# Kernel optimization log

Hardware: AMD Instinct MI355X
Metric: run time of the kernel (lower is better)

Reference implementation:

```python
import jax, jax.numpy as jnp
import numpy as np

N, E, D = 40000, 640000, 128
EPS = 1e-5


def _lin(k, out_d, in_d):
    s = 1.0 / np.sqrt(in_d)
    kw, kb = jax.random.split(k)
    W = jax.random.uniform(kw, (out_d, in_d), minval=-s, maxval=s, dtype=jnp.float32)
    b = jax.random.uniform(kb, (out_d,), minval=-s, maxval=s, dtype=jnp.float32)
    return W, b


def setup_inputs() -> dict:
    key = jax.random.key(0)
    kx, ke, k1, k2, k3, k4 = jax.random.split(key, 6)
    x = jax.random.normal(kx, (N, D), dtype=jnp.float32)
    edge_index = jax.random.randint(ke, (2, E), 0, N, dtype=jnp.int64)
    Wm1, bm1 = _lin(k1, D, D)
    Wm2, bm2 = _lin(k2, D, D)
    Wu1, bu1 = _lin(k3, D, 2 * D)
    Wu2, bu2 = _lin(k4, D, D)
    gamma = jnp.ones((D,), jnp.float32)
    beta = jnp.zeros((D,), jnp.float32)
    return dict(x=x, edge_index=edge_index, Wm1=Wm1, bm1=bm1, Wm2=Wm2, bm2=bm2,
                Wu1=Wu1, bu1=bu1, Wu2=Wu2, bu2=bu2, gamma=gamma, beta=beta)


def reference(x, edge_index, Wm1, bm1, Wm2, bm2, Wu1, bu1, Wu2, bu2, gamma, beta):
    num_nodes = x.shape[0]
    src, dst = edge_index[0], edge_index[1]
    # message MLP on gathered source features: (E, D)
    m = jax.nn.relu(x[src] @ Wm1.T + bm1) @ Wm2.T + bm2
    # scatter-mean via segment_sum + clamped count
    agg = jax.ops.segment_sum(m, dst, num_segments=num_nodes)
    cnt = jax.ops.segment_sum(jnp.ones((dst.shape[0],), m.dtype), dst, num_segments=num_nodes)
    agg = agg / jnp.clip(cnt, 1.0, None)[:, None]
    # update MLP on concat([x, agg]) -> (N, D); dropout is identity in eval
    comb = jnp.concatenate([x, agg], axis=-1)
    u = jax.nn.relu(comb @ Wu1.T + bu1) @ Wu2.T + bu2
    # residual + LayerNorm
    h = u + x
    mu = h.mean(-1, keepdims=True)
    var = ((h - mu) ** 2).mean(-1, keepdims=True)
    return (h - mu) / jnp.sqrt(var + EPS) * gamma + beta
```

## Files before the change

kernel.cpp:

```cpp
#include <hip/hip_runtime.h>

#define N_NODES 40000
#define N_EDGES 640000
#define DIM 128
#define PAD 64
#define NBLK_GEMM 313

typedef __bf16 bf16;
typedef __bf16 v8bf __attribute__((ext_vector_type(8)));
typedef __bf16 v4bf __attribute__((ext_vector_type(4)));
typedef float f32x4 __attribute__((ext_vector_type(4)));

#define MFMA(a, b, c) __builtin_amdgcn_mfma_f32_16x16x32_bf16(a, b, c, 0, 0, 0)

#define OFF_WM1 0
#define OFF_BM1 16384
#define OFF_WM2 16512
#define OFF_BM2 32896
#define OFF_WU1 33024
#define OFF_BU1 65792
#define OFF_WU2 65920
#define OFF_BU2 82304
#define OFF_GAM 82432
#define OFF_BET 82560
#define NPARAM  82688

__global__ __launch_bounds__(256) void front_kernel(
    const void* __restrict__ x, const void* __restrict__ ei,
    const void* p0, const void* p1, const void* p2, const void* p3,
    const void* p4, const void* p5, const void* p6, const void* p7,
    const void* p8, const void* p9,
    bf16* __restrict__ wp, bf16* __restrict__ xb,
    int* __restrict__ cnt, int* __restrict__ flags)
{
    __shared__ int sf[2];
    const int tid = threadIdx.x;
    const int gid = blockIdx.x * 256 + tid;
    const int gstride = gridDim.x * 256;

    if (tid == 0) { sf[0] = 0; sf[1] = 0; }
    __syncthreads();
    {
        const unsigned short* xh = (const unsigned short*)x;
        const unsigned int* eiw = (const unsigned int*)ei;
        int isf32 = 0; unsigned int orhi = 0;
        #pragma unroll
        for (int j = 0; j < 4; ++j) {
            unsigned short h = xh[2 * (tid + 256 * j)];
            if (((h >> 7) & 0xFF) >= 0xC0) isf32 = 1;
            orhi |= eiw[2 * (tid + 256 * j) + 1];
        }
        if (isf32) atomicOr(&sf[0], 1);
        if (orhi)  atomicOr(&sf[1], 1);
    }
    __syncthreads();
    const int f32m = sf[0];
    if (blockIdx.x == 0 && tid == 0) { flags[0] = f32m; flags[1] = sf[1] ? 0 : 1; }

    for (int i = gid; i < NPARAM; i += gstride) {
        const void* src; int base;
        if      (i < OFF_BM1) { src = p0; base = OFF_WM1; }
        else if (i < OFF_WM2) { src = p1; base = OFF_BM1; }
        else if (i < OFF_BM2) { src = p2; base = OFF_WM2; }
        else if (i < OFF_WU1) { src = p3; base = OFF_BM2; }
        else if (i < OFF_BU1) { src = p4; base = OFF_WU1; }
        else if (i < OFF_WU2) { src = p5; base = OFF_BU1; }
        else if (i < OFF_BU2) { src = p6; base = OFF_WU2; }
        else if (i < OFF_GAM) { src = p7; base = OFF_BU2; }
        else if (i < OFF_BET) { src = p8; base = OFF_GAM; }
        else                  { src = p9; base = OFF_BET; }
        int j = i - base;
        float v = f32m ? ((const float*)src)[j] : (float)((const bf16*)src)[j];
        wp[i] = (bf16)v;
    }
    {
        const int NT = N_NODES * DIM;
        if (f32m) {
            const float4* g = (const float4*)x;
            v4bf* o = (v4bf*)xb;
            for (int i = gid; i < NT / 4; i += gstride) {
                float4 v = g[i];
                v4bf t; t[0] = (bf16)v.x; t[1] = (bf16)v.y; t[2] = (bf16)v.z; t[3] = (bf16)v.w;
                o[i] = t;
            }
        } else {
            const uint4* g = (const uint4*)x;
            uint4* o = (uint4*)xb;
            for (int i = gid; i < NT / 8; i += gstride) o[i] = g[i];
        }
    }
    for (int i = gid; i < N_NODES; i += gstride) cnt[i] = 0;
}

__global__ __launch_bounds__(256) void scatter_kernel(const void* __restrict__ ei,
                                                      int* __restrict__ cnt,
                                                      int* __restrict__ padded,
                                                      const int* __restrict__ flags) {
    int e = blockIdx.x * 256 + threadIdx.x;
    if (e >= N_EDGES) return;
    int s, d;
    if (flags[1]) {
        const long long* p = (const long long*)ei;
        s = (int)p[e]; d = (int)p[N_EDGES + e];
    } else {
        const int* p = (const int*)ei;
        s = p[e]; d = p[N_EDGES + e];
    }
    int pos = atomicAdd(&cnt[d], 1);
    if (pos < PAD) padded[(d << 6) + pos] = s;
}

__global__ __launch_bounds__(256) void msg_kernel(const bf16* __restrict__ xb,
                                                  const bf16* __restrict__ wp,
                                                  bf16* __restrict__ y)
{
    __shared__ __align__(16) bf16 sc[4][32 * DIM];
    const int wave = threadIdx.x >> 6, lane = threadIdx.x & 63;
    const int l15 = lane & 15, quad = lane >> 4;
    const int row0 = (blockIdx.x * 4 + wave) * 32;
    bf16* s = sc[wave];
    const bf16* W1 = wp + OFF_WM1;
    const bf16* W2 = wp + OFF_WM2;

    const int ra = min(row0 + l15, N_NODES - 1);
    const int rb = min(row0 + 16 + l15, N_NODES - 1);

    f32x4 acc[2][8] = {};
    #pragma unroll
    for (int kt = 0; kt < 4; ++kt) {
        int k0 = kt * 32 + quad * 8;
        v8bf a0 = *(const v8bf*)&xb[(size_t)ra * DIM + k0];
        v8bf a1 = *(const v8bf*)&xb[(size_t)rb * DIM + k0];
        #pragma unroll
        for (int ct = 0; ct < 8; ++ct) {
            v8bf b = *(const v8bf*)&W1[(ct * 16 + l15) * DIM + k0];
            acc[0][ct] = MFMA(a0, b, acc[0][ct]);
            acc[1][ct] = MFMA(a1, b, acc[1][ct]);
        }
    }
    #pragma unroll
    for (int ct = 0; ct < 8; ++ct) {
        float bb = (float)wp[OFF_BM1 + ct * 16 + l15];
        int c8w = (ct << 1) | (l15 >> 3);
        #pragma unroll
        for (int i = 0; i < 2; ++i)
            #pragma unroll
            for (int r = 0; r < 4; ++r) {
                int row = i * 16 + quad * 4 + r;
                s[row * DIM + (((c8w ^ (row & 15)) << 3) | (l15 & 7))] =
                    (bf16)fmaxf(acc[i][ct][r] + bb, 0.f);
            }
    }
    f32x4 acc2[2][8] = {};
    #pragma unroll
    for (int kt = 0; kt < 4; ++kt) {
        int k0 = kt * 32 + quad * 8;
        int c8 = kt * 4 + quad;
        v8bf a0 = *(const v8bf*)&s[l15 * DIM + ((c8 ^ l15) << 3)];
        v8bf a1 = *(const v8bf*)&s[(16 + l15) * DIM + ((c8 ^ l15) << 3)];
        #pragma unroll
        for (int ct = 0; ct < 8; ++ct) {
            v8bf b = *(const v8bf*)&W2[(ct * 16 + l15) * DIM + k0];
            acc2[0][ct] = MFMA(a0, b, acc2[0][ct]);
            acc2[1][ct] = MFMA(a1, b, acc2[1][ct]);
        }
    }
    #pragma unroll
    for (int ct = 0; ct < 8; ++ct) {
        float bb = (float)wp[OFF_BM2 + ct * 16 + l15];
        #pragma unroll
        for (int i = 0; i < 2; ++i)
            #pragma unroll
            for (int r = 0; r < 4; ++r) {
                int grow = row0 + i * 16 + quad * 4 + r;
                if (grow < N_NODES)
                    y[(size_t)grow * DIM + ct * 16 + l15] = (bf16)(acc2[i][ct][r] + bb);
            }
    }
}

__global__ __launch_bounds__(256) void update_kernel(const bf16* __restrict__ xb,
                                                     const bf16* __restrict__ agg,
                                                     const bf16* __restrict__ wp,
                                                     const int* __restrict__ flags,
                                                     void* __restrict__ out)
{
    __shared__ __align__(16) bf16 sc[4][32 * DIM];
    const int wave = threadIdx.x >> 6, lane = threadIdx.x & 63;
    const int l15 = lane & 15, quad = lane >> 4;
    const int row0 = (blockIdx.x * 4 + wave) * 32;
    bf16* s = sc[wave];
    const bf16* W1 = wp + OFF_WU1;
    const bf16* W2 = wp + OFF_WU2;
    const int of32 = flags[0];

    const int ra = min(row0 + l15, N_NODES - 1);
    const int rb = min(row0 + 16 + l15, N_NODES - 1);

    f32x4 acc[2][8] = {};
    #pragma unroll
    for (int kt = 0; kt < 8; ++kt) {
        int k0 = kt * 32 + quad * 8;
        const bf16* A = (kt < 4) ? xb : agg;
        int ko = (kt < 4) ? k0 : (k0 - 128);
        v8bf a0 = *(const v8bf*)&A[(size_t)ra * DIM + ko];
        v8bf a1 = *(const v8bf*)&A[(size_t)rb * DIM + ko];
        #pragma unroll
        for (int ct = 0; ct < 8; ++ct) {
            v8bf b = *(const v8bf*)&W1[(ct * 16 + l15) * 256 + k0];
            acc[0][ct] = MFMA(a0, b, acc[0][ct]);
            acc[1][ct] = MFMA(a1, b, acc[1][ct]);
        }
    }
    #pragma unroll
    for (int ct = 0; ct < 8; ++ct) {
        float bb = (float)wp[OFF_BU1 + ct * 16 + l15];
        int c8w = (ct << 1) | (l15 >> 3);
        #pragma unroll
        for (int i = 0; i < 2; ++i)
            #pragma unroll
            for (int r = 0; r < 4; ++r) {
                int row = i * 16 + quad * 4 + r;
                s[row * DIM + (((c8w ^ (row & 15)) << 3) | (l15 & 7))] =
                    (bf16)fmaxf(acc[i][ct][r] + bb, 0.f);
            }
    }
    f32x4 acc2[2][8] = {};
    #pragma unroll
    for (int kt = 0; kt < 4; ++kt) {
        int k0 = kt * 32 + quad * 8;
        int c8 = kt * 4 + quad;
        v8bf a0 = *(const v8bf*)&s[l15 * DIM + ((c8 ^ l15) << 3)];
        v8bf a1 = *(const v8bf*)&s[(16 + l15) * DIM + ((c8 ^ l15) << 3)];
        #pragma unroll
        for (int ct = 0; ct < 8; ++ct) {
            v8bf b = *(const v8bf*)&W2[(ct * 16 + l15) * DIM + k0];
            acc2[0][ct] = MFMA(a0, b, acc2[0][ct]);
            acc2[1][ct] = MFMA(a1, b, acc2[1][ct]);
        }
    }

    float bu2c[8], gc[8], bc[8];
    #pragma unroll
    for (int ct = 0; ct < 8; ++ct) {
        int col = ct * 16 + l15;
        bu2c[ct] = (float)wp[OFF_BU2 + col];
        gc[ct]   = (float)wp[OFF_GAM + col];
        bc[ct]   = (float)wp[OFF_BET + col];
    }
    #pragma unroll
    for (int i = 0; i < 2; ++i) {
        #pragma unroll
        for (int r = 0; r < 4; ++r) {
            int grow = row0 + i * 16 + quad * 4 + r;
            int growc = min(grow, N_NODES - 1);
            float u[8], s1 = 0.f, s2 = 0.f;
            #pragma unroll
            for (int ct = 0; ct < 8; ++ct) {
                float v = acc2[i][ct][r] + bu2c[ct]
                        + (float)xb[(size_t)growc * DIM + ct * 16 + l15];
                u[ct] = v; s1 += v; s2 += v * v;
            }
            #pragma unroll
            for (int off = 1; off < 16; off <<= 1) {
                s1 += __shfl_xor(s1, off);
                s2 += __shfl_xor(s2, off);
            }
            float mean = s1 * (1.f / 128.f);
            float var  = s2 * (1.f / 128.f) - mean * mean;
            float rstd = rsqrtf(var + 1e-5f);
            if (grow < N_NODES) {
                if (of32) {
                    #pragma unroll
                    for (int ct = 0; ct < 8; ++ct)
                        ((float*)out)[(size_t)grow * DIM + ct * 16 + l15] =
                            (u[ct] - mean) * rstd * gc[ct] + bc[ct];
                } else {
                    #pragma unroll
                    for (int ct = 0; ct < 8; ++ct)
                        ((bf16*)out)[(size_t)grow * DIM + ct * 16 + l15] =
                            (bf16)((u[ct] - mean) * rstd * gc[ct] + bc[ct]);
                }
            }
        }
    }
}

__device__ __forceinline__ void accum8(float* s, uint4 v) {
    v8bf b = __builtin_bit_cast(v8bf, v);
    #pragma unroll
    for (int j = 0; j < 8; ++j) s[j] += (float)b[j];
}

__global__ __launch_bounds__(256) void agg_kernel(const bf16* __restrict__ y,
                                                  const int* __restrict__ padded,
                                                  const int* __restrict__ cnt,
                                                  bf16* __restrict__ agg) {
    const int node = (blockIdx.x << 2) + (threadIdx.x >> 6);
    const int lane = threadIdx.x & 63;
    const int slot = lane >> 4, c16 = lane & 15;
    const int c = min(cnt[node], PAD);
    const int beg = node << 6;
    const int end = beg + c;
    const uint4* yv = (const uint4*)y;

    float s0[8] = {}, s1[8] = {};
    int e = beg + slot;
    for (; e + 4 < end; e += 8) {
        int i0 = padded[e], i1 = padded[e + 4];
        uint4 v0 = yv[(size_t)i0 * 16 + c16];
        uint4 v1 = yv[(size_t)i1 * 16 + c16];
        accum8(s0, v0);
        accum8(s1, v1);
    }
    if (e < end) accum8(s0, yv[(size_t)padded[e] * 16 + c16]);

    float inv = 1.f / (float)(c > 0 ? c : 1);
    v8bf o;
    #pragma unroll
    for (int j = 0; j < 8; ++j) {
        float v = s0[j] + s1[j];
        v += __shfl_xor(v, 16);
        v += __shfl_xor(v, 32);
        o[j] = (bf16)(v * inv);
    }
    if (slot == 0)
        ((uint4*)agg)[(size_t)node * 16 + c16] = __builtin_bit_cast(uint4, o);
}

extern "C" void kernel_launch(void* const* d_in, const int* in_sizes, int n_in,
                              void* d_out, int out_size, void* d_ws, size_t ws_size,
                              hipStream_t stream) {
    const void* x  = d_in[0];
    const void* ei = d_in[1];

    char* ws = (char*)d_ws;
    size_t off = 0;
    auto alloc = [&](size_t bytes) {
        void* p = ws + off;
        off += (bytes + 255) & ~(size_t)255;
        return p;
    };
    bf16* y      = (bf16*)alloc((size_t)N_NODES * DIM * sizeof(bf16));
    bf16* agg    = (bf16*)alloc((size_t)N_NODES * DIM * sizeof(bf16));
    bf16* xb     = (bf16*)alloc((size_t)N_NODES * DIM * sizeof(bf16));
    bf16* wp     = (bf16*)alloc((size_t)NPARAM * sizeof(bf16));
    int*  cnt    = (int*)alloc(N_NODES * sizeof(int));
    int*  padded = (int*)alloc((size_t)N_NODES * PAD * sizeof(int));
    int*  flags  = (int*)alloc(256);

    front_kernel<<<1024, 256, 0, stream>>>(
        x, ei, d_in[2], d_in[3], d_in[4], d_in[5], d_in[6], d_in[7],
        d_in[8], d_in[9], d_in[10], d_in[11], wp, xb, cnt, flags);
    scatter_kernel<<<(N_EDGES + 255) / 256, 256, 0, stream>>>(ei, cnt, padded, flags);
    msg_kernel<<<NBLK_GEMM, 256, 0, stream>>>(xb, wp, y);
    agg_kernel<<<N_NODES / 4, 256, 0, stream>>>(y, padded, cnt, agg);
    update_kernel<<<NBLK_GEMM, 256, 0, stream>>>(xb, agg, wp, flags, d_out);
}
```

Before: 221.3 us.

## Fuse edge scatter with message MLP and drop the bf16 pre-conversion kernel

```diff
diff --git a/kernel.cpp b/kernel.cpp
--- a/kernel.cpp
+++ b/kernel.cpp
@@ -4,124 +4,63 @@
 #define N_EDGES 640000
 #define DIM 128
 #define PAD 64
-#define NBLK_GEMM 313
+#define NBLK_MSG 313
+#define FAT_BLOCKS (NBLK_MSG * 9)
 
 typedef __bf16 bf16;
 typedef __bf16 v8bf __attribute__((ext_vector_type(8)));
-typedef __bf16 v4bf __attribute__((ext_vector_type(4)));
 typedef float f32x4 __attribute__((ext_vector_type(4)));
 
 #define MFMA(a, b, c) __builtin_amdgcn_mfma_f32_16x16x32_bf16(a, b, c, 0, 0, 0)
 
-#define OFF_WM1 0
-#define OFF_BM1 16384
-#define OFF_WM2 16512
-#define OFF_BM2 32896
-#define OFF_WU1 33024
-#define OFF_BU1 65792
-#define OFF_WU2 65920
-#define OFF_BU2 82304
-#define OFF_GAM 82432
-#define OFF_BET 82560
-#define NPARAM  82688
-
-__global__ __launch_bounds__(256) void front_kernel(
-    const void* __restrict__ x, const void* __restrict__ ei,
-    const void* p0, const void* p1, const void* p2, const void* p3,
-    const void* p4, const void* p5, const void* p6, const void* p7,
-    const void* p8, const void* p9,
-    bf16* __restrict__ wp, bf16* __restrict__ xb,
-    int* __restrict__ cnt, int* __restrict__ flags)
-{
-    __shared__ int sf[2];
+__device__ __forceinline__ void detect(const void* x, const void* ei,
+                                       int* sf, int& f32m, int& i64m) {
     const int tid = threadIdx.x;
-    const int gid = blockIdx.x * 256 + tid;
-    const int gstride = gridDim.x * 256;
-
     if (tid == 0) { sf[0] = 0; sf[1] = 0; }
     __syncthreads();
-    {
-        const unsigned short* xh = (const unsigned short*)x;
-        const unsigned int* eiw = (const unsigned int*)ei;
-        int isf32 = 0; unsigned int orhi = 0;
-        #pragma unroll
-        for (int j = 0; j < 4; ++j) {
-            unsigned short h = xh[2 * (tid + 256 * j)];
-            if (((h >> 7) & 0xFF) >= 0xC0) isf32 = 1;
-            orhi |= eiw[2 * (tid + 256 * j) + 1];
-        }
-        if (isf32) atomicOr(&sf[0], 1);
-        if (orhi)  atomicOr(&sf[1], 1);
-    }
+    const unsigned short* xh = (const unsigned short*)x;
+    const unsigned int* eiw = (const unsigned int*)ei;
+    int isf32 = 0; unsigned int orhi = 0;
+    #pragma unroll
+    for (int j = 0; j < 4; ++j) {
+        unsigned short h = xh[2 * (tid + 256 * j)];
+        if (((h >> 7) & 0xFF) >= 0xC0) isf32 = 1;
+        orhi |= eiw[2 * (tid + 256 * j) + 1];
+    }
+    if (isf32) atomicOr(&sf[0], 1);
+    if (orhi)  atomicOr(&sf[1], 1);
     __syncthreads();
-    const int f32m = sf[0];
-    if (blockIdx.x == 0 && tid == 0) { flags[0] = f32m; flags[1] = sf[1] ? 0 : 1; }
-
-    for (int i = gid; i < NPARAM; i += gstride) {
-        const void* src; int base;
-        if      (i < OFF_BM1) { src = p0; base = OFF_WM1; }
-        else if (i < OFF_WM2) { src = p1; base = OFF_BM1; }
-        else if (i < OFF_BM2) { src = p2; base = OFF_WM2; }
-        else if (i < OFF_WU1) { src = p3; base = OFF_BM2; }
-        else if (i < OFF_BU1) { src = p4; base = OFF_WU1; }
-        else if (i < OFF_WU2) { src = p5; base = OFF_BU1; }
-        else if (i < OFF_BU2) { src = p6; base = OFF_WU2; }
-        else if (i < OFF_GAM) { src = p7; base = OFF_BU2; }
-        else if (i < OFF_BET) { src = p8; base = OFF_GAM; }
-        else                  { src = p9; base = OFF_BET; }
-        int j = i - base;
-        float v = f32m ? ((const float*)src)[j] : (float)((const bf16*)src)[j];
-        wp[i] = (bf16)v;
-    }
-    {
-        const int NT = N_NODES * DIM;
-        if (f32m) {
-            const float4* g = (const float4*)x;
-            v4bf* o = (v4bf*)xb;
-            for (int i = gid; i < NT / 4; i += gstride) {
-                float4 v = g[i];
-                v4bf t; t[0] = (bf16)v.x; t[1] = (bf16)v.y; t[2] = (bf16)v.z; t[3] = (bf16)v.w;
-                o[i] = t;
-            }
-        } else {
-            const uint4* g = (const uint4*)x;
-            uint4* o = (uint4*)xb;
-            for (int i = gid; i < NT / 8; i += gstride) o[i] = g[i];
-        }
-    }
-    for (int i = gid; i < N_NODES; i += gstride) cnt[i] = 0;
-}
-
-__global__ __launch_bounds__(256) void scatter_kernel(const void* __restrict__ ei,
-                                                      int* __restrict__ cnt,
-                                                      int* __restrict__ padded,
-                                                      const int* __restrict__ flags) {
-    int e = blockIdx.x * 256 + threadIdx.x;
-    if (e >= N_EDGES) return;
-    int s, d;
-    if (flags[1]) {
-        const long long* p = (const long long*)ei;
-        s = (int)p[e]; d = (int)p[N_EDGES + e];
+    f32m = sf[0];
+    i64m = sf[1] ? 0 : 1;
+}
+
+template<bool F32>
+__device__ __forceinline__ v8bf ld8(const void* p, size_t idx) {
+    if constexpr (F32) {
+        const float* f = (const float*)p + idx;
+        float4 a = *(const float4*)f, b = *(const float4*)(f + 4);
+        v8bf r;
+        r[0] = (bf16)a.x; r[1] = (bf16)a.y; r[2] = (bf16)a.z; r[3] = (bf16)a.w;
+        r[4] = (bf16)b.x; r[5] = (bf16)b.y; r[6] = (bf16)b.z; r[7] = (bf16)b.w;
+        return r;
     } else {
-        const int* p = (const int*)ei;
-        s = p[e]; d = p[N_EDGES + e];
-    }
-    int pos = atomicAdd(&cnt[d], 1);
-    if (pos < PAD) padded[(d << 6) + pos] = s;
-}
-
-__global__ __launch_bounds__(256) void msg_kernel(const bf16* __restrict__ xb,
-                                                  const bf16* __restrict__ wp,
-                                                  bf16* __restrict__ y)
-{
-    __shared__ __align__(16) bf16 sc[4][32 * DIM];
+        return *(const v8bf*)((const bf16*)p + idx);
+    }
+}
+
+template<bool F32>
+__device__ __forceinline__ float lds1(const void* p, size_t i) {
+    if constexpr (F32) return ((const float*)p)[i];
+    else               return (float)((const bf16*)p)[i];
+}
+
+template<bool F32>
+__device__ void msg_body(const void* x, const void* Wm1, const void* bm1,
+                         const void* Wm2, const void* bm2,
+                         bf16* __restrict__ y, bf16* s, int mb) {
     const int wave = threadIdx.x >> 6, lane = threadIdx.x & 63;
     const int l15 = lane & 15, quad = lane >> 4;
-    const int row0 = (blockIdx.x * 4 + wave) * 32;
-    bf16* s = sc[wave];
-    const bf16* W1 = wp + OFF_WM1;
-    const bf16* W2 = wp + OFF_WM2;
-
+    const int row0 = (mb * 4 + wave) * 32;
     const int ra = min(row0 + l15, N_NODES - 1);
     const int rb = min(row0 + 16 + l15, N_NODES - 1);
 
@@ -129,18 +68,18 @@
     #pragma unroll
     for (int kt = 0; kt < 4; ++kt) {
         int k0 = kt * 32 + quad * 8;
-        v8bf a0 = *(const v8bf*)&xb[(size_t)ra * DIM + k0];
-        v8bf a1 = *(const v8bf*)&xb[(size_t)rb * DIM + k0];
+        v8bf a0 = ld8<F32>(x, (size_t)ra * DIM + k0);
+        v8bf a1 = ld8<F32>(x, (size_t)rb * DIM + k0);
         #pragma unroll
         for (int ct = 0; ct < 8; ++ct) {
-            v8bf b = *(const v8bf*)&W1[(ct * 16 + l15) * DIM + k0];
+            v8bf b = ld8<F32>(Wm1, (size_t)(ct * 16 + l15) * DIM + k0);
             acc[0][ct] = MFMA(a0, b, acc[0][ct]);
             acc[1][ct] = MFMA(a1, b, acc[1][ct]);
         }
     }
     #pragma unroll
     for (int ct = 0; ct < 8; ++ct) {
-        float bb = (float)wp[OFF_BM1 + ct * 16 + l15];
+        float bb = lds1<F32>(bm1, ct * 16 + l15);
         int c8w = (ct << 1) | (l15 >> 3);
         #pragma unroll
         for (int i = 0; i < 2; ++i)
@@ -160,14 +99,14 @@
         v8bf a1 = *(const v8bf*)&s[(16 + l15) * DIM + ((c8 ^ l15) << 3)];
         #pragma unroll
         for (int ct = 0; ct < 8; ++ct) {
-            v8bf b = *(const v8bf*)&W2[(ct * 16 + l15) * DIM + k0];
+            v8bf b = ld8<F32>(Wm2, (size_t)(ct * 16 + l15) * DIM + k0);
             acc2[0][ct] = MFMA(a0, b, acc2[0][ct]);
             acc2[1][ct] = MFMA(a1, b, acc2[1][ct]);
         }
     }
     #pragma unroll
     for (int ct = 0; ct < 8; ++ct) {
-        float bb = (float)wp[OFF_BM2 + ct * 16 + l15];
+        float bb = lds1<F32>(bm2, ct * 16 + l15);
         #pragma unroll
         for (int i = 0; i < 2; ++i)
             #pragma unroll
@@ -179,109 +118,36 @@
     }
 }
 
-__global__ __launch_bounds__(256) void update_kernel(const bf16* __restrict__ xb,
-                                                     const bf16* __restrict__ agg,
-                                                     const bf16* __restrict__ wp,
-                                                     const int* __restrict__ flags,
-                                                     void* __restrict__ out)
+__global__ __launch_bounds__(256) void fat_kernel(
+    const void* __restrict__ x, const void* __restrict__ ei,
+    const void* Wm1, const void* bm1, const void* Wm2, const void* bm2,
+    int* __restrict__ cnt, unsigned short* __restrict__ padded,
+    bf16* __restrict__ y)
 {
     __shared__ __align__(16) bf16 sc[4][32 * DIM];
-    const int wave = threadIdx.x >> 6, lane = threadIdx.x & 63;
-    const int l15 = lane & 15, quad = lane >> 4;
-    const int row0 = (blockIdx.x * 4 + wave) * 32;
-    bf16* s = sc[wave];
-    const bf16* W1 = wp + OFF_WU1;
-    const bf16* W2 = wp + OFF_WU2;
-    const int of32 = flags[0];
-
-    const int ra = min(row0 + l15, N_NODES - 1);
-    const int rb = min(row0 + 16 + l15, N_NODES - 1);
-
-    f32x4 acc[2][8] = {};
-    #pragma unroll
-    for (int kt = 0; kt < 8; ++kt) {
-        int k0 = kt * 32 + quad * 8;
-        const bf16* A = (kt < 4) ? xb : agg;
-        int ko = (kt < 4) ? k0 : (k0 - 128);
-        v8bf a0 = *(const v8bf*)&A[(size_t)ra * DIM + ko];
-        v8bf a1 = *(const v8bf*)&A[(size_t)rb * DIM + ko];
-        #pragma unroll
-        for (int ct = 0; ct < 8; ++ct) {
-            v8bf b = *(const v8bf*)&W1[(ct * 16 + l15) * 256 + k0];
-            acc[0][ct] = MFMA(a0, b, acc[0][ct]);
-            acc[1][ct] = MFMA(a1, b, acc[1][ct]);
-        }
-    }
-    #pragma unroll
-    for (int ct = 0; ct < 8; ++ct) {
-        float bb = (float)wp[OFF_BU1 + ct * 16 + l15];
-        int c8w = (ct << 1) | (l15 >> 3);
-        #pragma unroll
-        for (int i = 0; i < 2; ++i)
-            #pragma unroll
-            for (int r = 0; r < 4; ++r) {
-                int row = i * 16 + quad * 4 + r;
-                s[row * DIM + (((c8w ^ (row & 15)) << 3) | (l15 & 7))] =
-                    (bf16)fmaxf(acc[i][ct][r] + bb, 0.f);
-            }
-    }
-    f32x4 acc2[2][8] = {};
-    #pragma unroll
-    for (int kt = 0; kt < 4; ++kt) {
-        int k0 = kt * 32 + quad * 8;
-        int c8 = kt * 4 + quad;
-        v8bf a0 = *(const v8bf*)&s[l15 * DIM + ((c8 ^ l15) << 3)];
-        v8bf a1 = *(const v8bf*)&s[(16 + l15) * DIM + ((c8 ^ l15) << 3)];
-        #pragma unroll
-        for (int ct = 0; ct < 8; ++ct) {
-            v8bf b = *(const v8bf*)&W2[(ct * 16 + l15) * DIM + k0];
-            acc2[0][ct] = MFMA(a0, b, acc2[0][ct]);
-            acc2[1][ct] = MFMA(a1, b, acc2[1][ct]);
-        }
-    }
-
-    float bu2c[8], gc[8], bc[8];
-    #pragma unroll
-    for (int ct = 0; ct < 8; ++ct) {
-        int col = ct * 16 + l15;
-        bu2c[ct] = (float)wp[OFF_BU2 + col];
-        gc[ct]   = (float)wp[OFF_GAM + col];
-        bc[ct]   = (float)wp[OFF_BET + col];
-    }
-    #pragma unroll
-    for (int i = 0; i < 2; ++i) {
-        #pragma unroll
-        for (int r = 0; r < 4; ++r) {
-            int grow = row0 + i * 16 + quad * 4 + r;
-            int growc = min(grow, N_NODES - 1);
-            float u[8], s1 = 0.f, s2 = 0.f;
-            #pragma unroll
-            for (int ct = 0; ct < 8; ++ct) {
-                float v = acc2[i][ct][r] + bu2c[ct]
-                        + (float)xb[(size_t)growc * DIM + ct * 16 + l15];
-                u[ct] = v; s1 += v; s2 += v * v;
-            }
-            #pragma unroll
-            for (int off = 1; off < 16; off <<= 1) {
-                s1 += __shfl_xor(s1, off);
-                s2 += __shfl_xor(s2, off);
-            }
-            float mean = s1 * (1.f / 128.f);
-            float var  = s2 * (1.f / 128.f) - mean * mean;
-            float rstd = rsqrtf(var + 1e-5f);
-            if (grow < N_NODES) {
-                if (of32) {
-                    #pragma unroll
-                    for (int ct = 0; ct < 8; ++ct)
-                        ((float*)out)[(size_t)grow * DIM + ct * 16 + l15] =
-                            (u[ct] - mean) * rstd * gc[ct] + bc[ct];
-                } else {
-                    #pragma unroll
-                    for (int ct = 0; ct < 8; ++ct)
-                        ((bf16*)out)[(size_t)grow * DIM + ct * 16 + l15] =
-                            (bf16)((u[ct] - mean) * rstd * gc[ct] + bc[ct]);
-                }
-            }
+    __shared__ int sf[2];
+    int f32m, i64m;
+    detect(x, ei, sf, f32m, i64m);
+
+    const int bx = blockIdx.x;
+    if (bx % 9 == 0) {
+        int mb = bx / 9;
+        if (f32m) msg_body<true>(x, Wm1, bm1, Wm2, bm2, y, sc[threadIdx.x >> 6], mb);
+        else      msg_body<false>(x, Wm1, bm1, Wm2, bm2, y, sc[threadIdx.x >> 6], mb);
+    } else {
+        int sb = bx - bx / 9 - 1;
+        int e = sb * 256 + threadIdx.x;
+        if (e < N_EDGES) {
+            int s, d;
+            if (i64m) {
+                const long long* p = (const long long*)ei;
+                s = (int)p[e]; d = (int)p[N_EDGES + e];
+            } else {
+                const int* p = (const int*)ei;
+                s = p[e]; d = p[N_EDGES + e];
+            }
+            int pos = atomicAdd(&cnt[d], 1);
+            if (pos < PAD) padded[(d << 6) + pos] = (unsigned short)s;
         }
     }
 }
@@ -293,7 +159,7 @@
 }
 
 __global__ __launch_bounds__(256) void agg_kernel(const bf16* __restrict__ y,
-                                                  const int* __restrict__ padded,
+                                                  const unsigned short* __restrict__ padded,
                                                   const int* __restrict__ cnt,
                                                   bf16* __restrict__ agg) {
     const int node = (blockIdx.x << 2) + (threadIdx.x >> 6);
@@ -328,6 +194,122 @@
         ((uint4*)agg)[(size_t)node * 16 + c16] = __builtin_bit_cast(uint4, o);
 }
 
+template<bool F32>
+__device__ void update_body(const void* x, const bf16* __restrict__ agg,
+                            const void* Wu1, const void* bu1,
+                            const void* Wu2, const void* bu2,
+                            const void* gam, const void* bet,
+                            void* __restrict__ out, bf16* s, int ub) {
+    const int wave = threadIdx.x >> 6, lane = threadIdx.x & 63;
+    const int l15 = lane & 15, quad = lane >> 4;
+    const int row0 = (ub * 4 + wave) * 32;
+    const int ra = min(row0 + l15, N_NODES - 1);
+    const int rb = min(row0 + 16 + l15, N_NODES - 1);
+
+    f32x4 acc[2][8] = {};
+    #pragma unroll
+    for (int kt = 0; kt < 8; ++kt) {
+        int k0 = kt * 32 + quad * 8;
+        v8bf a0, a1;
+        if (kt < 4) {
+            a0 = ld8<F32>(x, (size_t)ra * DIM + k0);
+            a1 = ld8<F32>(x, (size_t)rb * DIM + k0);
+        } else {
+            a0 = *(const v8bf*)&agg[(size_t)ra * DIM + (k0 - 128)];
+            a1 = *(const v8bf*)&agg[(size_t)rb * DIM + (k0 - 128)];
+        }
+        #pragma unroll
+        for (int ct = 0; ct < 8; ++ct) {
+            v8bf b = ld8<F32>(Wu1, (size_t)(ct * 16 + l15) * 256 + k0);
+            acc[0][ct] = MFMA(a0, b, acc[0][ct]);
+            acc[1][ct] = MFMA(a1, b, acc[1][ct]);
+        }
+    }
+    #pragma unroll
+    for (int ct = 0; ct < 8; ++ct) {
+        float bb = lds1<F32>(bu1, ct * 16 + l15);
+        int c8w = (ct << 1) | (l15 >> 3);
+        #pragma unroll
+        for (int i = 0; i < 2; ++i)
+            #pragma unroll
+            for (int r = 0; r < 4; ++r) {
+                int row = i * 16 + quad * 4 + r;
+                s[row * DIM + (((c8w ^ (row & 15)) << 3) | (l15 & 7))] =
+                    (bf16)fmaxf(acc[i][ct][r] + bb, 0.f);
+            }
+    }
+    f32x4 acc2[2][8] = {};
+    #pragma unroll
+    for (int kt = 0; kt < 4; ++kt) {
+        int k0 = kt * 32 + quad * 8;
+        int c8 = kt * 4 + quad;
+        v8bf a0 = *(const v8bf*)&s[l15 * DIM + ((c8 ^ l15) << 3)];
+        v8bf a1 = *(const v8bf*)&s[(16 + l15) * DIM + ((c8 ^ l15) << 3)];
+        #pragma unroll
+        for (int ct = 0; ct < 8; ++ct) {
+            v8bf b = ld8<F32>(Wu2, (size_t)(ct * 16 + l15) * DIM + k0);
+            acc2[0][ct] = MFMA(a0, b, acc2[0][ct]);
+            acc2[1][ct] = MFMA(a1, b, acc2[1][ct]);
+        }
+    }
+
+    float bu2c[8], gc[8], bc[8];
+    #pragma unroll
+    for (int ct = 0; ct < 8; ++ct) {
+        int col = ct * 16 + l15;
+        bu2c[ct] = lds1<F32>(bu2, col);
+        gc[ct]   = lds1<F32>(gam, col);
+        bc[ct]   = lds1<F32>(bet, col);
+    }
+    #pragma unroll
+    for (int i = 0; i < 2; ++i) {
+        #pragma unroll
+        for (int r = 0; r < 4; ++r) {
+            int grow = row0 + i * 16 + quad * 4 + r;
+            size_t growc = (size_t)min(grow, N_NODES - 1);
+            float u[8], s1 = 0.f, s2 = 0.f;
+            #pragma unroll
+            for (int ct = 0; ct < 8; ++ct) {
+                float v = acc2[i][ct][r] + bu2c[ct]
+                        + lds1<F32>(x, growc * DIM + ct * 16 + l15);
+                u[ct] = v; s1 += v; s2 += v * v;
+            }
+            #pragma unroll
+            for (int off = 1; off < 16; off <<= 1) {
+                s1 += __shfl_xor(s1, off);
+                s2 += __shfl_xor(s2, off);
+            }
+            float mean = s1 * (1.f / 128.f);
+            float var  = s2 * (1.f / 128.f) - mean * mean;
+            float rstd = rsqrtf(var + 1e-5f);
+            if (grow < N_NODES) {
+                #pragma unroll
+                for (int ct = 0; ct < 8; ++ct) {
+                    float v = (u[ct] - mean) * rstd * gc[ct] + bc[ct];
+                    if constexpr (F32) ((float*)out)[(size_t)grow * DIM + ct * 16 + l15] = v;
+                    else               ((bf16*)out)[(size_t)grow * DIM + ct * 16 + l15] = (bf16)v;
+                }
+            }
+        }
+    }
+}
+
+__global__ __launch_bounds__(256) void update_kernel(
+    const void* __restrict__ x, const void* __restrict__ ei,
+    const bf16* __restrict__ agg,
+    const void* Wu1, const void* bu1, const void* Wu2, const void* bu2,
+    const void* gam, const void* bet, void* __restrict__ out)
+{
+    __shared__ __align__(16) bf16 sc[4][32 * DIM];
+    __shared__ int sf[2];
+    int f32m, i64m;
+    detect(x, ei, sf, f32m, i64m);
+    if (f32m) update_body<true>(x, agg, Wu1, bu1, Wu2, bu2, gam, bet, out,
+                                sc[threadIdx.x >> 6], blockIdx.x);
+    else      update_body<false>(x, agg, Wu1, bu1, Wu2, bu2, gam, bet, out,
+                                 sc[threadIdx.x >> 6], blockIdx.x);
+}
+
 extern "C" void kernel_launch(void* const* d_in, const int* in_sizes, int n_in,
                               void* d_out, int out_size, void* d_ws, size_t ws_size,
                               hipStream_t stream) {
@@ -341,19 +323,17 @@
         off += (bytes + 255) & ~(size_t)255;
         return p;
     };
-    bf16* y      = (bf16*)alloc((size_t)N_NODES * DIM * sizeof(bf16));
-    bf16* agg    = (bf16*)alloc((size_t)N_NODES * DIM * sizeof(bf16));
-    bf16* xb     = (bf16*)alloc((size_t)N_NODES * DIM * sizeof(bf16));
-    bf16* wp     = (bf16*)alloc((size_t)NPARAM * sizeof(bf16));
-    int*  cnt    = (int*)alloc(N_NODES * sizeof(int));
-    int*  padded = (int*)alloc((size_t)N_NODES * PAD * sizeof(int));
-    int*  flags  = (int*)alloc(256);
-
-    front_kernel<<<1024, 256, 0, stream>>>(
-        x, ei, d_in[2], d_in[3], d_in[4], d_in[5], d_in[6], d_in[7],
-        d_in[8], d_in[9], d_in[10], d_in[11], wp, xb, cnt, flags);
-    scatter_kernel<<<(N_EDGES + 255) / 256, 256, 0, stream>>>(ei, cnt, padded, flags);
-    msg_kernel<<<NBLK_GEMM, 256, 0, stream>>>(xb, wp, y);
+    bf16* y   = (bf16*)alloc((size_t)N_NODES * DIM * sizeof(bf16));
+    bf16* agg = (bf16*)alloc((size_t)N_NODES * DIM * sizeof(bf16));
+    int*  cnt = (int*)alloc(N_NODES * sizeof(int));
+    unsigned short* padded =
+        (unsigned short*)alloc((size_t)N_NODES * PAD * sizeof(unsigned short));
+
+    hipMemsetAsync(cnt, 0, N_NODES * sizeof(int), stream);
+
+    fat_kernel<<<FAT_BLOCKS, 256, 0, stream>>>(
+        x, ei, d_in[2], d_in[3], d_in[4], d_in[5], cnt, padded, y);
     agg_kernel<<<N_NODES / 4, 256, 0, stream>>>(y, padded, cnt, agg);
-    update_kernel<<<NBLK_GEMM, 256, 0, stream>>>(xb, agg, wp, flags, d_out);
-}
+    update_kernel<<<NBLK_MSG, 256, 0, stream>>>(
+        x, ei, agg, d_in[6], d_in[7], d_in[8], d_in[9], d_in[10], d_in[11], d_out);
+}
```

After: 250.7 us. 13.3% more time.
